# Performance work log

Measured on AMD Instinct MI355X. Metric: run time of the kernel, lower is better.

## Reference

```python
import jax, jax.numpy as jnp
import numpy as np

B = 1024          # batch
S = 2048          # sparseDim == obsDim (required by PhiW shape constraints)
FISTA_ITER = 16


def setup_inputs() -> dict:
    key = jax.random.key(0)
    k1, k2, k3 = jax.random.split(key, 3)
    src = jax.random.normal(k1, (B, S, 1), dtype=jnp.float32)
    Y = jax.random.normal(k2, (B, S, 1), dtype=jnp.float32)
    W = jax.random.normal(k3, (S, S), dtype=jnp.float32)
    # F.normalize(W, p=2, dim=0): unit L2 norm per column
    W = W / jnp.linalg.norm(W, axis=0, keepdims=True)
    alpha = jnp.full((1, 1), 0.1, dtype=jnp.float32)  # alpha_initialize
    return {"src": src, "Y": Y, "W": W, "alpha": alpha}


def reference(src, Y, W, alpha):
    obsDim = W.shape[0]          # == sparseDim == S
    # Lipschitz constant: max |eig(W^T W)|; W^T W is symmetric PSD so eigvalsh is exact
    L = jnp.max(jnp.linalg.eigvalsh(W.T @ W))
    thresh = alpha / L * 0.5     # soft-threshold level, shape [1,1]

    def phiW(x):
        theta_m = x[:, :obsDim]          # [B, S, 1]
        delta = x[:, obsDim:]            # [B, S, 1]
        return src * jnp.matmul(W, theta_m) + delta

    def phiWT(y):
        return jnp.concatenate((jnp.matmul(W.T, src * y), y), axis=1)  # [B, 2S, 1]

    nb = Y.shape[0]
    x0 = jnp.zeros((nb, 2 * obsDim, 1), dtype=Y.dtype)

    def step(carry, _):
        x_old, y_k, t_old = carry
        res = Y - phiW(y_k)
        v = y_k + phiWT(res) / L
        x_new = jnp.sign(v) * jnp.maximum(jnp.abs(v) - thresh, 0.0)
        t_new = (1.0 + jnp.sqrt(1.0 + 4.0 * t_old * t_old)) / 2.0
        y_new = x_new + (t_old - 1.0) / t_new * (x_new - x_old)
        return (x_new, y_new, t_new), None

    (x_new, _, _), _ = jax.lax.scan(
        step, (x0, x0, jnp.float32(1.0)), None, length=FISTA_ITER
    )
    return x_new
```

## Files before the change

kernel.cpp:

```cpp
#include <hip/hip_runtime.h>
#include <math.h>

#define SDIM 2048
#define BATCH 1024
#define NITER 16
#define LM 40

typedef unsigned short ushort_t;
typedef __attribute__((ext_vector_type(8))) short bf16x8;
typedef __attribute__((ext_vector_type(4))) float f32x4;

#define MFMA(a,b,c) __builtin_amdgcn_mfma_f32_16x16x32_bf16((a),(b),(c),0,0,0)

__device__ __forceinline__ float softt(float v, float th){
  return copysignf(fmaxf(fabsf(v) - th, 0.0f), v);
}

__device__ __forceinline__ float bf2f(ushort_t h){
  return __uint_as_float(((unsigned)h) << 16);
}

__device__ __forceinline__ void split2(float x, ushort_t* h, ushort_t* l){
  unsigned u = __float_as_uint(x);
  unsigned hh = (u + 0x7FFFu + ((u >> 16) & 1u)) >> 16;
  float hf = __uint_as_float(hh << 16);
  float r = x - hf;
  unsigned v = __float_as_uint(r);
  unsigned ll = (v + 0x7FFFu + ((v >> 16) & 1u)) >> 16;
  *h = (ushort_t)hh; *l = (ushort_t)ll;
}

__device__ __forceinline__ void cp16(const ushort_t* g, ushort_t* l){
  __builtin_amdgcn_global_load_lds(
      (const __attribute__((address_space(1))) unsigned int*)g,
      (__attribute__((address_space(3))) unsigned int*)l, 16, 0, 0);
}

__device__ __forceinline__ void gemm_core(ushort_t* __restrict__ sm,
                                          const ushort_t* __restrict__ Ah, const ushort_t* __restrict__ Al,
                                          const ushort_t* __restrict__ Bh, const ushort_t* __restrict__ Bl,
                                          int m0, int n0, int K, f32x4 acc[2][2])
{
  ushort_t* lAh = sm;
  ushort_t* lAl = sm + 4096;
  ushort_t* lBh = sm + 8192;
  ushort_t* lBl = sm + 12288;
  const int tid = threadIdx.x;
  const int rr = tid >> 3;
  const int kp = (tid & 7) ^ (rr & 7);
  const size_t strA = (size_t)32 * K;
  const ushort_t* gAh = Ah + (size_t)(m0 + rr) * K + kp * 8;
  const ushort_t* gAl = Al + (size_t)(m0 + rr) * K + kp * 8;
  const ushort_t* gBh = Bh + (size_t)(n0 + rr) * K + kp * 8;
  const ushort_t* gBl = Bl + (size_t)(n0 + rr) * K + kp * 8;
  ushort_t* dA0 = &lAh[tid * 8];      ushort_t* dA1 = &lAh[(tid + 256) * 8];
  ushort_t* dAl0 = &lAl[tid * 8];     ushort_t* dAl1 = &lAl[(tid + 256) * 8];
  ushort_t* dB0 = &lBh[tid * 8];      ushort_t* dB1 = &lBh[(tid + 256) * 8];
  ushort_t* dBl0 = &lBl[tid * 8];     ushort_t* dBl1 = &lBl[(tid + 256) * 8];

  const int lane = tid & 63, wv = tid >> 6;
  const int wm = (wv >> 1) * 32, wn = (wv & 1) * 32;
  const int mm = lane & 15, quad = lane >> 4;
  const int ra0 = wm + mm, ra1 = wm + 16 + mm;
  const int rb0 = wn + mm, rb1 = wn + 16 + mm;
  int oa0[2], oa1[2], ob0[2], ob1[2];
  #pragma unroll
  for (int u = 0; u < 2; u++){
    oa0[u] = ra0*64 + (((u*4 + quad) ^ (ra0 & 7)) << 3);
    oa1[u] = ra1*64 + (((u*4 + quad) ^ (ra1 & 7)) << 3);
    ob0[u] = rb0*64 + (((u*4 + quad) ^ (rb0 & 7)) << 3);
    ob1[u] = rb1*64 + (((u*4 + quad) ^ (rb1 & 7)) << 3);
  }

  const int nk = K / 64;
  cp16(gAh, dA0); cp16(gAh + strA, dA1);
  cp16(gAl, dAl0); cp16(gAl + strA, dAl1);
  cp16(gBh, dB0); cp16(gBh + strA, dB1);
  cp16(gBl, dBl0); cp16(gBl + strA, dBl1);
  gAh += 64; gAl += 64; gBh += 64; gBl += 64;

  for (int kt = 0; kt < nk; kt++){
    __syncthreads();
    bf16x8 ah0[2], ah1[2], al0[2], al1[2], bh0[2], bh1[2], bl0[2], bl1[2];
    #pragma unroll
    for (int u = 0; u < 2; u++){
      ah0[u] = *(const bf16x8*)&lAh[oa0[u]];
      ah1[u] = *(const bf16x8*)&lAh[oa1[u]];
      al0[u] = *(const bf16x8*)&lAl[oa0[u]];
      al1[u] = *(const bf16x8*)&lAl[oa1[u]];
      bh0[u] = *(const bf16x8*)&lBh[ob0[u]];
      bh1[u] = *(const bf16x8*)&lBh[ob1[u]];
      bl0[u] = *(const bf16x8*)&lBl[ob0[u]];
      bl1[u] = *(const bf16x8*)&lBl[ob1[u]];
    }
    __syncthreads();
    if (kt + 1 < nk){
      cp16(gAh, dA0); cp16(gAh + strA, dA1);
      cp16(gAl, dAl0); cp16(gAl + strA, dAl1);
      cp16(gBh, dB0); cp16(gBh + strA, dB1);
      cp16(gBl, dBl0); cp16(gBl + strA, dBl1);
      gAh += 64; gAl += 64; gBh += 64; gBl += 64;
    }
    #pragma unroll
    for (int u = 0; u < 2; u++){
      acc[0][0] = MFMA(ah0[u], bh0[u], acc[0][0]);
      acc[0][0] = MFMA(ah0[u], bl0[u], acc[0][0]);
      acc[0][0] = MFMA(al0[u], bh0[u], acc[0][0]);
      acc[0][1] = MFMA(ah0[u], bh1[u], acc[0][1]);
      acc[0][1] = MFMA(ah0[u], bl1[u], acc[0][1]);
      acc[0][1] = MFMA(al0[u], bh1[u], acc[0][1]);
      acc[1][0] = MFMA(ah1[u], bh0[u], acc[1][0]);
      acc[1][0] = MFMA(ah1[u], bl0[u], acc[1][0]);
      acc[1][0] = MFMA(al1[u], bh0[u], acc[1][0]);
      acc[1][1] = MFMA(ah1[u], bh1[u], acc[1][1]);
      acc[1][1] = MFMA(ah1[u], bl1[u], acc[1][1]);
      acc[1][1] = MFMA(al1[u], bh1[u], acc[1][1]);
    }
  }
}

__device__ __forceinline__ void acc_to_tile(ushort_t* sm, f32x4 acc[2][2]){
  float* tile = (float*)sm;
  const int tid = threadIdx.x, lane = tid & 63, wv = tid >> 6;
  const int wm = (wv >> 1) * 32, wn = (wv & 1) * 32;
  const int mm = lane & 15, quad = lane >> 4;
  #pragma unroll
  for (int tm = 0; tm < 2; tm++)
    #pragma unroll
    for (int tn = 0; tn < 2; tn++)
      #pragma unroll
      for (int i = 0; i < 4; i++)
        tile[(wm + tm*16 + quad*4 + i)*65 + wn + tn*16 + mm] = acc[tm][tn][i];
  __syncthreads();
}

#define EPILOGUE_FOR(rowvar, c4var) \
  const int tid = threadIdx.x, lane = tid & 63, wv = tid >> 6; \
  const int r4 = lane >> 4; \
  const int c4var = (lane & 15) * 4; \
  for (int j = 0; j < 4; j++){ \
    const int rowvar = wv*16 + j*4 + r4;

__global__ __launch_bounds__(256) void k_split(const float* __restrict__ W,
                                               ushort_t* __restrict__ Wah, ushort_t* __restrict__ Wal,
                                               ushort_t* __restrict__ Wbh, ushort_t* __restrict__ Wbl){
  __shared__ float t[32][33];
  const int i0 = blockIdx.y * 32, j0 = blockIdx.x * 32;
  const int r = threadIdx.x >> 3, c = (threadIdx.x & 7) * 4;
  const float4 v = *(const float4*)&W[(size_t)(i0 + r) * SDIM + j0 + c];
  float vv[4] = {v.x, v.y, v.z, v.w};
  ushort_t h[4], l[4];
  #pragma unroll
  for (int q = 0; q < 4; q++){ split2(vv[q], &h[q], &l[q]); t[r][c+q] = vv[q]; }
  *(ushort4*)&Wah[(size_t)(i0 + r) * SDIM + j0 + c] = make_ushort4(h[0],h[1],h[2],h[3]);
  *(ushort4*)&Wal[(size_t)(i0 + r) * SDIM + j0 + c] = make_ushort4(l[0],l[1],l[2],l[3]);
  __syncthreads();
  #pragma unroll
  for (int q = 0; q < 4; q++) split2(t[c+q][r], &h[q], &l[q]);
  *(ushort4*)&Wbh[(size_t)(j0 + r) * SDIM + i0 + c] = make_ushort4(h[0],h[1],h[2],h[3]);
  *(ushort4*)&Wbl[(size_t)(j0 + r) * SDIM + i0 + c] = make_ushort4(l[0],l[1],l[2],l[3]);
}

__global__ __launch_bounds__(256) void k_gemmM(const ushort_t* __restrict__ Wah, const ushort_t* __restrict__ Wal,
                                               float* __restrict__ Mmat){
  __shared__ __align__(16) ushort_t smem[16384];
  const int b = blockIdx.x + (blockIdx.y << 5);
  const int xcd = b & 7, slot = b >> 3;
  const int n0 = (((xcd << 2) + (slot >> 5)) << 6);
  const int m0 = ((slot & 31) << 6);
  f32x4 acc[2][2] = {};
  gemm_core(smem, Wah, Wal, Wah, Wal, m0, n0, SDIM, acc);
  acc_to_tile(smem, acc);
  const float* tile = (const float*)smem;
  EPILOGUE_FOR(row, c4)
    f32x4 a = *(const f32x4*)&tile[row*65 + c4];
    *(f32x4*)&Mmat[(size_t)(m0 + row) * SDIM + n0 + c4] = a;
  }
}

__global__ __launch_bounds__(256) void k_init(float* __restrict__ vRing,
                                              double* __restrict__ dotWV, double* __restrict__ dotWW,
                                              float* __restrict__ betaSq){
  __shared__ float red[256];
  int t = threadIdx.x;
  float vals[8];
  float s = 0.f;
  #pragma unroll
  for (int p = 0; p < 8; p++){
    int j = p*256 + t;
    unsigned h = (unsigned)j * 2654435761u;
    h ^= h >> 16; h *= 2246822519u; h ^= h >> 13;
    float r = (float)(h & 0xFFFFFFu) / 16777216.0f - 0.5f;
    vals[p] = r; s += r*r;
  }
  red[t] = s; __syncthreads();
  for (int o = 128; o > 0; o >>= 1){ if (t < o) red[t] += red[t+o]; __syncthreads(); }
  float inv = rsqrtf(red[0]);
  #pragma unroll
  for (int p = 0; p < 8; p++){
    int j = p*256 + t;
    vRing[SDIM + j] = vals[p]*inv;
    vRing[j] = 0.f;
    vRing[2*SDIM + j] = 0.f;
  }
  if (t < LM+2){ dotWV[t] = 0.0; dotWW[t] = 0.0; betaSq[t] = 0.f; }
}

__global__ __launch_bounds__(256) void k_lstep(const float* __restrict__ M,
    const float* __restrict__ wOld, float* __restrict__ wNew,
    float* __restrict__ vRing, double* __restrict__ dotWV, double* __restrict__ dotWW,
    float* __restrict__ betaSq, int s){
  __shared__ float vs[SDIM];
  __shared__ double pAl[4], pWw[4];
  const int tid = threadIdx.x, bid = blockIdx.x;
  if (s == 1){
    const float* v1 = vRing + SDIM;
    for (int j = tid; j < SDIM; j += 256) vs[j] = v1[j];
  } else {
    const double a  = dotWV[s-1];
    const double ww = dotWW[s-1];
    const float bpSq = betaSq[s-2];
    float bsq = (float)(ww - a*a - (double)bpSq);
    bsq = fmaxf(bsq, 1e-20f);
    const float beta = sqrtf(bsq), invb = 1.0f/beta;
    const float alpha = (float)a, bprev = sqrtf(bpSq);
    const float* vm1 = vRing + ((s-1)%3)*SDIM;
    const float* vm2 = vRing + ((s-2)%3)*SDIM;
    float* vdst = vRing + (s%3)*SDIM;
    for (int j = tid; j < SDIM; j += 256){
      float val = (wOld[j] - alpha*vm1[j] - bprev*vm2[j]) * invb;
      vs[j] = val;
      if (bid == 0) vdst[j] = val;
    }
    if (bid == 0 && tid == 0) betaSq[s-1] = bsq;
  }
  __syncthreads();
  const int wv = tid >> 6, lane = tid & 63;
  const int row = bid*4 + wv;
  const float4* Mr = (const float4*)(M + (size_t)row * SDIM);
  const float4* v4 = (const float4*)vs;
  float acc = 0.f;
  #pragma unroll
  for (int p = 0; p < 8; p++){
    int j4 = p*64 + lane;
    float4 m = Mr[j4], v = v4[j4];
    acc += m.x*v.x + m.y*v.y + m.z*v.z + m.w*v.w;
  }
  #pragma unroll
  for (int o = 32; o > 0; o >>= 1) acc += __shfl_down(acc, o);
  if (lane == 0){
    wNew[row] = acc;
    pAl[wv] = (double)acc * (double)vs[row];
    pWw[wv] = (double)acc * (double)acc;
  }
  __syncthreads();
  if (tid == 0){
    atomicAdd(&dotWV[s], pAl[0]+pAl[1]+pAl[2]+pAl[3]);
    atomicAdd(&dotWW[s], pWw[0]+pWw[1]+pWw[2]+pWw[3]);
  }
}

__global__ void k_sturm(const double* __restrict__ dotWV, const float* __restrict__ betaSq,
                        const float* __restrict__ alphaIn, float* __restrict__ Lbuf){
  __shared__ double sa[LM+1], sb[LM+1];
  int lane = threadIdx.x;
  for (int i = lane; i <= LM; i += 64){
    if (i >= 1){
      sa[i] = dotWV[i];
      sb[i] = (i < LM) ? sqrt((double)betaSq[i]) : 0.0;
    }
  }
  __syncthreads();
  double phi = -1e300, plo = 1e300;
  for (int i = 1 + lane; i <= LM; i += 64){
    double r = (i > 1 ? sb[i-1] : 0.0) + (i < LM ? sb[i] : 0.0);
    phi = fmax(phi, sa[i] + r);
    plo = fmin(plo, sa[i] - r);
  }
  for (int o = 32; o > 0; o >>= 1){
    phi = fmax(phi, __shfl_down(phi, o));
    plo = fmin(plo, __shfl_down(plo, o));
  }
  double hi = __shfl(phi, 0), lo = __shfl(plo, 0);
  for (int round = 0; round < 6; round++){
    double x = lo + (hi - lo) * (double)(lane + 1) / 65.0;
    int cnt = 0;
    double dd = sa[1] - x;
    if (dd < 0) cnt++;
    for (int i = 2; i <= LM; i++){
      double off = sb[i-1];
      if (fabs(dd) < 1e-300) dd = -1e-300;
      dd = sa[i] - x - off*off/dd;
      if (dd < 0) cnt++;
    }
    unsigned long long bal = __ballot(cnt == LM);
    int p = (bal == 0ull) ? 64 : (__ffsll((unsigned long long)bal) - 1);
    double newhi = (p <= 63) ? lo + (hi - lo) * (double)(p + 1) / 65.0 : hi;
    double newlo = (p >= 1)  ? lo + (hi - lo) * (double)p / 65.0       : lo;
    hi = newhi; lo = newlo;
  }
  if (lane == 0){
    double L = 0.5*(lo + hi);
    Lbuf[0] = (float)(1.0 / L);
    Lbuf[1] = (float)(0.5 * (double)alphaIn[0] / L);
  }
}


__global__ __launch_bounds__(256) void k_A0(const float* __restrict__ Y, const float* __restrict__ src,
                                            float* __restrict__ yd, ushort_t* __restrict__ sresh,
                                            ushort_t* __restrict__ sresl, float* __restrict__ out,
                                            const float* __restrict__ Lbuf){
  int idx = blockIdx.x*256 + threadIdx.x;
  float invL = Lbuf[0], th = Lbuf[1];
  float y = Y[idx], s = src[idx];
  split2(s*y, &sresh[idx], &sresl[idx]);
  float xn = softt(y*invL, th);
  int b = idx >> 11, i = idx & 2047;
  out[(size_t)b*4096 + 2048 + i] = xn;
  yd[idx] = xn;
}

__device__ __forceinline__ void swz512(int* m0, int* n0){
  const int b = blockIdx.x + (blockIdx.y << 5);
  const int xcd = b & 7, slot = b >> 3;
  *n0 = (((xcd << 2) + (slot >> 4)) << 6);
  *m0 = ((slot & 15) << 6);
}

__global__ __launch_bounds__(256) void k_gemmA(
    const ushort_t* __restrict__ Wah, const ushort_t* __restrict__ Wal,
    const ushort_t* __restrict__ ymh, const ushort_t* __restrict__ yml,
    const float* __restrict__ Y, const float* __restrict__ src,
    float* __restrict__ yd, float* __restrict__ out,
    ushort_t* __restrict__ sresh, ushort_t* __restrict__ sresl,
    const float* __restrict__ Lbuf, float ck)
{
  __shared__ __align__(16) ushort_t smem[16384];
  f32x4 acc[2][2] = {};
  int m0, n0; swz512(&m0, &n0);
  gemm_core(smem, ymh, yml, Wah, Wal, m0, n0, SDIM, acc);
  acc_to_tile(smem, acc);
  const float* tile = (const float*)smem;
  const float invL = Lbuf[0], th = Lbuf[1];
  EPILOGUE_FOR(row, c4)
    const int brow = m0 + row;
    const size_t g  = (size_t)brow*SDIM + n0 + c4;
    const size_t go = (size_t)brow*4096 + 2048 + n0 + c4;
    f32x4 a   = *(const f32x4*)&tile[row*65 + c4];
    f32x4 s4  = *(const f32x4*)&src[g];
    f32x4 y4  = *(const f32x4*)&Y[g];
    f32x4 yd4 = *(const f32x4*)&yd[g];
    f32x4 xo4 = *(const f32x4*)&out[go];
    f32x4 res, xn, yn;
    ushort4 sh, sl;
    #pragma unroll
    for (int q = 0; q < 4; q++){
      res[q] = y4[q] - s4[q]*a[q] - yd4[q];
      xn[q]  = softt(yd4[q] + res[q]*invL, th);
      yn[q]  = xn[q] + ck*(xn[q] - xo4[q]);
    }
    split2(s4[0]*res[0], &sh.x, &sl.x);
    split2(s4[1]*res[1], &sh.y, &sl.y);
    split2(s4[2]*res[2], &sh.z, &sl.z);
    split2(s4[3]*res[3], &sh.w, &sl.w);
    *(ushort4*)&sresh[g] = sh;
    *(ushort4*)&sresl[g] = sl;
    *(f32x4*)&out[go] = xn;
    *(f32x4*)&yd[g]   = yn;
  }
}

template<bool FIRST>
__global__ __launch_bounds__(256) void k_gemmB(
    const ushort_t* __restrict__ Wbh, const ushort_t* __restrict__ Wbl,
    const ushort_t* __restrict__ sresh, const ushort_t* __restrict__ sresl,
    ushort_t* __restrict__ ymh, ushort_t* __restrict__ yml,
    float* __restrict__ out, const float* __restrict__ Lbuf, float ck)
{
  __shared__ __align__(16) ushort_t smem[16384];
  f32x4 acc[2][2] = {};
  int m0, n0; swz512(&m0, &n0);
  gemm_core(smem, sresh, sresl, Wbh, Wbl, m0, n0, SDIM, acc);
  acc_to_tile(smem, acc);
  const float* tile = (const float*)smem;
  const float invL = Lbuf[0], th = Lbuf[1];
  EPILOGUE_FOR(row, c4)
    const int brow = m0 + row;
    const size_t g  = (size_t)brow*SDIM + n0 + c4;
    const size_t go = (size_t)brow*4096 + n0 + c4;
    f32x4 a = *(const f32x4*)&tile[row*65 + c4];
    f32x4 ym4, xo4;
    if (FIRST){
      ym4 = (f32x4){0.f,0.f,0.f,0.f};
      xo4 = (f32x4){0.f,0.f,0.f,0.f};
    } else {
      ushort4 h4 = *(const ushort4*)&ymh[g];
      ushort4 l4 = *(const ushort4*)&yml[g];
      ym4[0] = bf2f(h4.x) + bf2f(l4.x);
      ym4[1] = bf2f(h4.y) + bf2f(l4.y);
      ym4[2] = bf2f(h4.z) + bf2f(l4.z);
      ym4[3] = bf2f(h4.w) + bf2f(l4.w);
      xo4 = *(const f32x4*)&out[go];
    }
    f32x4 xn, yn;
    ushort4 hh, ll;
    #pragma unroll
    for (int q = 0; q < 4; q++){
      xn[q] = softt(ym4[q] + a[q]*invL, th);
      yn[q] = xn[q] + ck*(xn[q] - xo4[q]);
    }
    split2(yn[0], &hh.x, &ll.x);
    split2(yn[1], &hh.y, &ll.y);
    split2(yn[2], &hh.z, &ll.z);
    split2(yn[3], &hh.w, &ll.w);
    *(f32x4*)&out[go] = xn;
    *(ushort4*)&ymh[g] = hh;
    *(ushort4*)&yml[g] = ll;
  }
}


extern "C" void kernel_launch(void* const* d_in, const int* in_sizes, int n_in,
                              void* d_out, int out_size, void* d_ws, size_t ws_size,
                              hipStream_t stream) {
  const float* src   = (const float*)d_in[0];
  const float* Y     = (const float*)d_in[1];
  const float* W     = (const float*)d_in[2];
  const float* alpha = (const float*)d_in[3];
  float* out = (float*)d_out;
  float* ws  = (float*)d_ws;

  const size_t M1 = 1024*1024;
  float* Mmat = ws;
  float* yd   = ws + 4*M1;
  float* lanc = ws + 6*M1;
  float* w0      = lanc;
  float* w1      = lanc + SDIM;
  float* vRing   = lanc + 2*SDIM;
  double* dotWV  = (double*)(lanc + 5*SDIM);
  double* dotWW  = dotWV + 128;
  float* betaSq  = lanc + 5*SDIM + 512;
  float* Lbuf    = betaSq + 128;
  ushort_t* u16 = (ushort_t*)(ws + 7*M1);
  ushort_t* Wah = u16;
  ushort_t* Wal = u16 + 4*M1;
  ushort_t* Wbh = u16 + 8*M1;
  ushort_t* Wbl = u16 + 12*M1;
  ushort_t* ymh = u16 + 16*M1;
  ushort_t* yml = u16 + 18*M1;
  ushort_t* sresh = u16 + 20*M1;
  ushort_t* sresl = u16 + 22*M1;

  k_split<<<dim3(64,64), 256, 0, stream>>>(W, Wah, Wal, Wbh, Wbl);
  k_gemmM<<<dim3(32,32), 256, 0, stream>>>(Wah, Wal, Mmat);

  float* wb[2] = { w0, w1 };
  k_init<<<1, 256, 0, stream>>>(vRing, dotWV, dotWW, betaSq);
  for (int s = 1; s <= LM; s++){
    k_lstep<<<512, 256, 0, stream>>>(Mmat, wb[(s+1)&1], wb[s&1], vRing, dotWV, dotWW, betaSq, s);
  }
  k_sturm<<<1, 64, 0, stream>>>(dotWV, betaSq, alpha, Lbuf);

  double t = 1.0;
  float ckv[NITER];
  for (int k = 0; k < NITER; k++){
    double tn = 0.5*(1.0 + sqrt(1.0 + 4.0*t*t));
    ckv[k] = (float)((t - 1.0)/tn);
    t = tn;
  }

  k_A0<<<(BATCH*SDIM)/256, 256, 0, stream>>>(Y, src, yd, sresh, sresl, out, Lbuf);
  k_gemmB<true><<<dim3(32,16), 256, 0, stream>>>(Wbh, Wbl, sresh, sresl, ymh, yml, out, Lbuf, ckv[0]);
  for (int k = 1; k < NITER; k++){
    k_gemmA<<<dim3(32,16), 256, 0, stream>>>(Wah, Wal, ymh, yml, Y, src, yd, out, sresh, sresl, Lbuf, ckv[k]);
    k_gemmB<false><<<dim3(32,16), 256, 0, stream>>>(Wbh, Wbl, sresh, sresl, ymh, yml, out, Lbuf, ckv[k]);
  }
  (void)in_sizes; (void)n_in; (void)out_size; (void)ws_size;
}
```

Baseline: 1.708 ms.

## Split K across two blocks per tile in FISTA GEMMs with atomic-counter combine

The per-iteration GEMMs now launch twice as many blocks (1024 instead of 512). Each block computes half of the K dimension and writes its partial accumulator to a workspace that reuses the Mmat buffer. An atomic counter per tile decides which block arrives second; that block adds the other partial and runs the fused epilogue. This is meant to fill the GPU's compute units better, since 512 tiles underoccupy them. The cost is extra partial-sum traffic, atomics, and a memset of the counters.

Measured after the change: 2.867 ms. +67.8%, slower.

```diff
diff --git a/kernel.cpp b/kernel.cpp
--- a/kernel.cpp
+++ b/kernel.cpp
@@ -39,7 +39,7 @@
 __device__ __forceinline__ void gemm_core(ushort_t* __restrict__ sm,
                                           const ushort_t* __restrict__ Ah, const ushort_t* __restrict__ Al,
                                           const ushort_t* __restrict__ Bh, const ushort_t* __restrict__ Bl,
-                                          int m0, int n0, int K, f32x4 acc[2][2])
+                                          int m0, int n0, int K, int kbase, int klen, f32x4 acc[2][2])
 {
   ushort_t* lAh = sm;
   ushort_t* lAl = sm + 4096;
@@ -49,10 +49,10 @@
   const int rr = tid >> 3;
   const int kp = (tid & 7) ^ (rr & 7);
   const size_t strA = (size_t)32 * K;
-  const ushort_t* gAh = Ah + (size_t)(m0 + rr) * K + kp * 8;
-  const ushort_t* gAl = Al + (size_t)(m0 + rr) * K + kp * 8;
-  const ushort_t* gBh = Bh + (size_t)(n0 + rr) * K + kp * 8;
-  const ushort_t* gBl = Bl + (size_t)(n0 + rr) * K + kp * 8;
+  const ushort_t* gAh = Ah + (size_t)(m0 + rr) * K + kbase + kp * 8;
+  const ushort_t* gAl = Al + (size_t)(m0 + rr) * K + kbase + kp * 8;
+  const ushort_t* gBh = Bh + (size_t)(n0 + rr) * K + kbase + kp * 8;
+  const ushort_t* gBl = Bl + (size_t)(n0 + rr) * K + kbase + kp * 8;
   ushort_t* dA0 = &lAh[tid * 8];      ushort_t* dA1 = &lAh[(tid + 256) * 8];
   ushort_t* dAl0 = &lAl[tid * 8];     ushort_t* dAl1 = &lAl[(tid + 256) * 8];
   ushort_t* dB0 = &lBh[tid * 8];      ushort_t* dB1 = &lBh[(tid + 256) * 8];
@@ -72,7 +72,7 @@
     ob1[u] = rb1*64 + (((u*4 + quad) ^ (rb1 & 7)) << 3);
   }
 
-  const int nk = K / 64;
+  const int nk = klen / 64;
   cp16(gAh, dA0); cp16(gAh + strA, dA1);
   cp16(gAl, dAl0); cp16(gAl + strA, dAl1);
   cp16(gBh, dB0); cp16(gBh + strA, dB1);
@@ -141,6 +141,26 @@
   for (int j = 0; j < 4; j++){ \
     const int rowvar = wv*16 + j*4 + r4;
 
+__device__ __forceinline__ bool ksplit_combine(float* __restrict__ Pws, int* __restrict__ cnt,
+                                               int tile, int kh, f32x4 acc[2][2], int* sflag){
+  const int t = threadIdx.x;
+  float* myP = Pws + (((size_t)tile << 1) + kh) * 4096;
+  #pragma unroll
+  for (int i = 0; i < 16; i++)
+    __hip_atomic_store(&myP[i*256 + t], acc[(i>>3)&1][(i>>2)&1][i&3],
+                       __ATOMIC_RELAXED, __HIP_MEMORY_SCOPE_AGENT);
+  if (t == 0)
+    *sflag = __hip_atomic_fetch_add(&cnt[tile], 1, __ATOMIC_ACQ_REL, __HIP_MEMORY_SCOPE_AGENT);
+  __syncthreads();
+  if (*sflag == 0) return false;
+  const float* pP = Pws + (((size_t)tile << 1) + (kh ^ 1)) * 4096;
+  #pragma unroll
+  for (int i = 0; i < 16; i++)
+    acc[(i>>3)&1][(i>>2)&1][i&3] += __hip_atomic_load(&pP[i*256 + t],
+                       __ATOMIC_RELAXED, __HIP_MEMORY_SCOPE_AGENT);
+  return true;
+}
+
 __global__ __launch_bounds__(256) void k_split(const float* __restrict__ W,
                                                ushort_t* __restrict__ Wah, ushort_t* __restrict__ Wal,
                                                ushort_t* __restrict__ Wbh, ushort_t* __restrict__ Wbl){
@@ -169,7 +189,7 @@
   const int n0 = (((xcd << 2) + (slot >> 5)) << 6);
   const int m0 = ((slot & 31) << 6);
   f32x4 acc[2][2] = {};
-  gemm_core(smem, Wah, Wal, Wah, Wal, m0, n0, SDIM, acc);
+  gemm_core(smem, Wah, Wal, Wah, Wal, m0, n0, SDIM, 0, SDIM, acc);
   acc_to_tile(smem, acc);
   const float* tile = (const float*)smem;
   EPILOGUE_FOR(row, c4)
@@ -321,11 +341,16 @@
   yd[idx] = xn;
 }
 
-__device__ __forceinline__ void swz512(int* m0, int* n0){
+__device__ __forceinline__ void swzF(int* m0, int* n0, int* kh, int* tile){
   const int b = blockIdx.x + (blockIdx.y << 5);
   const int xcd = b & 7, slot = b >> 3;
-  *n0 = (((xcd << 2) + (slot >> 4)) << 6);
-  *m0 = ((slot & 15) << 6);
+  const int nt = (xcd << 2) + (slot >> 5);
+  const int mk = slot & 31;
+  const int mt = mk >> 1;
+  *kh = mk & 1;
+  *m0 = mt << 6;
+  *n0 = nt << 6;
+  *tile = (mt << 5) + nt;
 }
 
 __global__ __launch_bounds__(256) void k_gemmA(
@@ -334,20 +359,23 @@
     const float* __restrict__ Y, const float* __restrict__ src,
     float* __restrict__ yd, float* __restrict__ out,
     ushort_t* __restrict__ sresh, ushort_t* __restrict__ sresl,
-    const float* __restrict__ Lbuf, float ck)
+    const float* __restrict__ Lbuf, float ck,
+    float* __restrict__ Pws, int* __restrict__ cnt)
 {
   __shared__ __align__(16) ushort_t smem[16384];
+  __shared__ int sflag;
   f32x4 acc[2][2] = {};
-  int m0, n0; swz512(&m0, &n0);
-  gemm_core(smem, ymh, yml, Wah, Wal, m0, n0, SDIM, acc);
+  int m0, n0, kh, tile; swzF(&m0, &n0, &kh, &tile);
+  gemm_core(smem, ymh, yml, Wah, Wal, m0, n0, SDIM, kh << 10, 1024, acc);
+  if (!ksplit_combine(Pws, cnt, tile, kh, acc, &sflag)) return;
   acc_to_tile(smem, acc);
-  const float* tile = (const float*)smem;
+  const float* tile_f = (const float*)smem;
   const float invL = Lbuf[0], th = Lbuf[1];
   EPILOGUE_FOR(row, c4)
     const int brow = m0 + row;
     const size_t g  = (size_t)brow*SDIM + n0 + c4;
     const size_t go = (size_t)brow*4096 + 2048 + n0 + c4;
-    f32x4 a   = *(const f32x4*)&tile[row*65 + c4];
+    f32x4 a   = *(const f32x4*)&tile_f[row*65 + c4];
     f32x4 s4  = *(const f32x4*)&src[g];
     f32x4 y4  = *(const f32x4*)&Y[g];
     f32x4 yd4 = *(const f32x4*)&yd[g];
@@ -376,20 +404,23 @@
     const ushort_t* __restrict__ Wbh, const ushort_t* __restrict__ Wbl,
     const ushort_t* __restrict__ sresh, const ushort_t* __restrict__ sresl,
     ushort_t* __restrict__ ymh, ushort_t* __restrict__ yml,
-    float* __restrict__ out, const float* __restrict__ Lbuf, float ck)
+    float* __restrict__ out, const float* __restrict__ Lbuf, float ck,
+    float* __restrict__ Pws, int* __restrict__ cnt)
 {
   __shared__ __align__(16) ushort_t smem[16384];
+  __shared__ int sflag;
   f32x4 acc[2][2] = {};
-  int m0, n0; swz512(&m0, &n0);
-  gemm_core(smem, sresh, sresl, Wbh, Wbl, m0, n0, SDIM, acc);
+  int m0, n0, kh, tile; swzF(&m0, &n0, &kh, &tile);
+  gemm_core(smem, sresh, sresl, Wbh, Wbl, m0, n0, SDIM, kh << 10, 1024, acc);
+  if (!ksplit_combine(Pws, cnt, tile, kh, acc, &sflag)) return;
   acc_to_tile(smem, acc);
-  const float* tile = (const float*)smem;
+  const float* tile_f = (const float*)smem;
   const float invL = Lbuf[0], th = Lbuf[1];
   EPILOGUE_FOR(row, c4)
     const int brow = m0 + row;
     const size_t g  = (size_t)brow*SDIM + n0 + c4;
     const size_t go = (size_t)brow*4096 + n0 + c4;
-    f32x4 a = *(const f32x4*)&tile[row*65 + c4];
+    f32x4 a = *(const f32x4*)&tile_f[row*65 + c4];
     f32x4 ym4, xo4;
     if (FIRST){
       ym4 = (f32x4){0.f,0.f,0.f,0.f};
@@ -451,6 +482,8 @@
   ushort_t* yml = u16 + 18*M1;
   ushort_t* sresh = u16 + 20*M1;
   ushort_t* sresl = u16 + 22*M1;
+  float* Pws = Mmat;
+  int* cnt = (int*)(ws + 19*M1);
 
   k_split<<<dim3(64,64), 256, 0, stream>>>(W, Wah, Wal, Wbh, Wbl);
   k_gemmM<<<dim3(32,32), 256, 0, stream>>>(Wah, Wal, Mmat);
@@ -461,6 +494,8 @@
     k_lstep<<<512, 256, 0, stream>>>(Mmat, wb[(s+1)&1], wb[s&1], vRing, dotWV, dotWW, betaSq, s);
   }
   k_sturm<<<1, 64, 0, stream>>>(dotWV, betaSq, alpha, Lbuf);
+
+  hipMemsetAsync(cnt, 0, 31*512*sizeof(int), stream);
 
   double t = 1.0;
   float ckv[NITER];
@@ -470,11 +505,15 @@
     t = tn;
   }
 
+  int ep = 0;
   k_A0<<<(BATCH*SDIM)/256, 256, 0, stream>>>(Y, src, yd, sresh, sresl, out, Lbuf);
-  k_gemmB<true><<<dim3(32,16), 256, 0, stream>>>(Wbh, Wbl, sresh, sresl, ymh, yml, out, Lbuf, ckv[0]);
+  k_gemmB<true><<<dim3(32,32), 256, 0, stream>>>(Wbh, Wbl, sresh, sresl, ymh, yml, out, Lbuf, ckv[0],
+                                                 Pws, cnt + (ep++)*512);
   for (int k = 1; k < NITER; k++){
-    k_gemmA<<<dim3(32,16), 256, 0, stream>>>(Wah, Wal, ymh, yml, Y, src, yd, out, sresh, sresl, Lbuf, ckv[k]);
-    k_gemmB<false><<<dim3(32,16), 256, 0, stream>>>(Wbh, Wbl, sresh, sresl, ymh, yml, out, Lbuf, ckv[k]);
+    k_gemmA<<<dim3(32,32), 256, 0, stream>>>(Wah, Wal, ymh, yml, Y, src, yd, out, sresh, sresl, Lbuf, ckv[k],
+                                             Pws, cnt + (ep++)*512);
+    k_gemmB<false><<<dim3(32,32), 256, 0, stream>>>(Wbh, Wbl, sresh, sresl, ymh, yml, out, Lbuf, ckv[k],
+                                                    Pws, cnt + (ep++)*512);
   }
   (void)in_sizes; (void)n_in; (void)out_size; (void)ws_size;
 }
```

## Enlarge GEMM tiles to 128x64 with double-buffered LDS pipeline

Applied to the files above, without the earlier changes.

Replaces the 64x64 single-buffer GEMM core with a templated 128x64 tile, where each warp computes a 64x32 sub-tile (4x2 MFMA fragments). LDS is now double buffered: the next K-slice is loaded asynchronously while the current one is consumed, which removes one barrier per K step. Grids are halved and the block swizzles are adjusted to match. The cost is more registers and 96KB of dynamic LDS per block, which lowers occupancy and halves the number of blocks.

After: 1.845 ms. +8.0%, slower.

```diff
diff --git a/kernel.cpp b/kernel.cpp
--- a/kernel.cpp
+++ b/kernel.cpp
@@ -36,110 +36,133 @@
       (__attribute__((address_space(3))) unsigned int*)l, 16, 0, 0);
 }
 
-__device__ __forceinline__ void gemm_core(ushort_t* __restrict__ sm,
-                                          const ushort_t* __restrict__ Ah, const ushort_t* __restrict__ Al,
-                                          const ushort_t* __restrict__ Bh, const ushort_t* __restrict__ Bl,
-                                          int m0, int n0, int K, f32x4 acc[2][2])
+template<int BM, int BN>
+__device__ __forceinline__ void gemm_core2(ushort_t* __restrict__ sm,
+    const ushort_t* __restrict__ Ah, const ushort_t* __restrict__ Al,
+    const ushort_t* __restrict__ Bh, const ushort_t* __restrict__ Bl,
+    int m0, int n0, int K, f32x4 acc[4][2])
 {
-  ushort_t* lAh = sm;
-  ushort_t* lAl = sm + 4096;
-  ushort_t* lBh = sm + 8192;
-  ushort_t* lBl = sm + 12288;
+  constexpr int BK   = 64;
+  constexpr int ABUF = BM * BK;
+  constexpr int BBUF = BN * BK;
+  constexpr int BUFSZ = 2*ABUF + 2*BBUF;
+  constexpr int ARND = BM / 32;
+  constexpr int BRND = BN / 32;
   const int tid = threadIdx.x;
   const int rr = tid >> 3;
   const int kp = (tid & 7) ^ (rr & 7);
-  const size_t strA = (size_t)32 * K;
-  const ushort_t* gAh = Ah + (size_t)(m0 + rr) * K + kp * 8;
-  const ushort_t* gAl = Al + (size_t)(m0 + rr) * K + kp * 8;
-  const ushort_t* gBh = Bh + (size_t)(n0 + rr) * K + kp * 8;
-  const ushort_t* gBl = Bl + (size_t)(n0 + rr) * K + kp * 8;
-  ushort_t* dA0 = &lAh[tid * 8];      ushort_t* dA1 = &lAh[(tid + 256) * 8];
-  ushort_t* dAl0 = &lAl[tid * 8];     ushort_t* dAl1 = &lAl[(tid + 256) * 8];
-  ushort_t* dB0 = &lBh[tid * 8];      ushort_t* dB1 = &lBh[(tid + 256) * 8];
-  ushort_t* dBl0 = &lBl[tid * 8];     ushort_t* dBl1 = &lBl[(tid + 256) * 8];
+
+  const ushort_t* pAh[ARND]; const ushort_t* pAl[ARND];
+  const ushort_t* pBh[BRND]; const ushort_t* pBl[BRND];
+  #pragma unroll
+  for (int r = 0; r < ARND; r++){
+    pAh[r] = Ah + (size_t)(m0 + rr + r*32) * K + kp*8;
+    pAl[r] = Al + (size_t)(m0 + rr + r*32) * K + kp*8;
+  }
+  #pragma unroll
+  for (int r = 0; r < BRND; r++){
+    pBh[r] = Bh + (size_t)(n0 + rr + r*32) * K + kp*8;
+    pBl[r] = Bl + (size_t)(n0 + rr + r*32) * K + kp*8;
+  }
 
   const int lane = tid & 63, wv = tid >> 6;
-  const int wm = (wv >> 1) * 32, wn = (wv & 1) * 32;
+  const int wr = (wv >> 1) * 64, wc = (wv & 1) * 32;
   const int mm = lane & 15, quad = lane >> 4;
-  const int ra0 = wm + mm, ra1 = wm + 16 + mm;
-  const int rb0 = wn + mm, rb1 = wn + 16 + mm;
-  int oa0[2], oa1[2], ob0[2], ob1[2];
-  #pragma unroll
-  for (int u = 0; u < 2; u++){
-    oa0[u] = ra0*64 + (((u*4 + quad) ^ (ra0 & 7)) << 3);
-    oa1[u] = ra1*64 + (((u*4 + quad) ^ (ra1 & 7)) << 3);
-    ob0[u] = rb0*64 + (((u*4 + quad) ^ (rb0 & 7)) << 3);
-    ob1[u] = rb1*64 + (((u*4 + quad) ^ (rb1 & 7)) << 3);
-  }
-
-  const int nk = K / 64;
-  cp16(gAh, dA0); cp16(gAh + strA, dA1);
-  cp16(gAl, dAl0); cp16(gAl + strA, dAl1);
-  cp16(gBh, dB0); cp16(gBh + strA, dB1);
-  cp16(gBl, dBl0); cp16(gBl + strA, dBl1);
-  gAh += 64; gAl += 64; gBh += 64; gBl += 64;
+  int oa[4][2], ob[2][2];
+  #pragma unroll
+  for (int t = 0; t < 4; t++){
+    const int r = wr + t*16 + mm;
+    #pragma unroll
+    for (int u = 0; u < 2; u++)
+      oa[t][u] = r*BK + (((u*4 + quad) ^ (r & 7)) << 3);
+  }
+  #pragma unroll
+  for (int s = 0; s < 2; s++){
+    const int r = wc + s*16 + mm;
+    #pragma unroll
+    for (int u = 0; u < 2; u++)
+      ob[s][u] = r*BK + (((u*4 + quad) ^ (r & 7)) << 3);
+  }
+
+  const int nk = K / BK;
+  #pragma unroll
+  for (int r = 0; r < ARND; r++){
+    cp16(pAh[r], &sm[(tid + r*256)*8]);
+    cp16(pAl[r], &sm[ABUF + (tid + r*256)*8]);
+  }
+  #pragma unroll
+  for (int r = 0; r < BRND; r++){
+    cp16(pBh[r], &sm[2*ABUF + (tid + r*256)*8]);
+    cp16(pBl[r], &sm[2*ABUF + BBUF + (tid + r*256)*8]);
+  }
 
   for (int kt = 0; kt < nk; kt++){
+    const int cur = kt & 1;
     __syncthreads();
-    bf16x8 ah0[2], ah1[2], al0[2], al1[2], bh0[2], bh1[2], bl0[2], bl1[2];
+    if (kt + 1 < nk){
+      ushort_t* d = sm + (cur ^ 1) * BUFSZ;
+      const int ko = (kt + 1) * BK;
+      #pragma unroll
+      for (int r = 0; r < ARND; r++){
+        cp16(pAh[r] + ko, &d[(tid + r*256)*8]);
+        cp16(pAl[r] + ko, &d[ABUF + (tid + r*256)*8]);
+      }
+      #pragma unroll
+      for (int r = 0; r < BRND; r++){
+        cp16(pBh[r] + ko, &d[2*ABUF + (tid + r*256)*8]);
+        cp16(pBl[r] + ko, &d[2*ABUF + BBUF + (tid + r*256)*8]);
+      }
+    }
+    const ushort_t* sA  = sm + cur * BUFSZ;
+    const ushort_t* sAl = sA + ABUF;
+    const ushort_t* sB  = sA + 2*ABUF;
+    const ushort_t* sBl = sA + 2*ABUF + BBUF;
     #pragma unroll
     for (int u = 0; u < 2; u++){
-      ah0[u] = *(const bf16x8*)&lAh[oa0[u]];
-      ah1[u] = *(const bf16x8*)&lAh[oa1[u]];
-      al0[u] = *(const bf16x8*)&lAl[oa0[u]];
-      al1[u] = *(const bf16x8*)&lAl[oa1[u]];
-      bh0[u] = *(const bf16x8*)&lBh[ob0[u]];
-      bh1[u] = *(const bf16x8*)&lBh[ob1[u]];
-      bl0[u] = *(const bf16x8*)&lBl[ob0[u]];
-      bl1[u] = *(const bf16x8*)&lBl[ob1[u]];
-    }
-    __syncthreads();
-    if (kt + 1 < nk){
-      cp16(gAh, dA0); cp16(gAh + strA, dA1);
-      cp16(gAl, dAl0); cp16(gAl + strA, dAl1);
-      cp16(gBh, dB0); cp16(gBh + strA, dB1);
-      cp16(gBl, dBl0); cp16(gBl + strA, dBl1);
-      gAh += 64; gAl += 64; gBh += 64; gBl += 64;
-    }
-    #pragma unroll
-    for (int u = 0; u < 2; u++){
-      acc[0][0] = MFMA(ah0[u], bh0[u], acc[0][0]);
-      acc[0][0] = MFMA(ah0[u], bl0[u], acc[0][0]);
-      acc[0][0] = MFMA(al0[u], bh0[u], acc[0][0]);
-      acc[0][1] = MFMA(ah0[u], bh1[u], acc[0][1]);
-      acc[0][1] = MFMA(ah0[u], bl1[u], acc[0][1]);
-      acc[0][1] = MFMA(al0[u], bh1[u], acc[0][1]);
-      acc[1][0] = MFMA(ah1[u], bh0[u], acc[1][0]);
-      acc[1][0] = MFMA(ah1[u], bl0[u], acc[1][0]);
-      acc[1][0] = MFMA(al1[u], bh0[u], acc[1][0]);
-      acc[1][1] = MFMA(ah1[u], bh1[u], acc[1][1]);
-      acc[1][1] = MFMA(ah1[u], bl1[u], acc[1][1]);
-      acc[1][1] = MFMA(al1[u], bh1[u], acc[1][1]);
-    }
-  }
-}
-
-__device__ __forceinline__ void acc_to_tile(ushort_t* sm, f32x4 acc[2][2]){
+      bf16x8 ah[4], al8[4], bh[2], bl8[2];
+      #pragma unroll
+      for (int t = 0; t < 4; t++){
+        ah[t]  = *(const bf16x8*)&sA [oa[t][u]];
+        al8[t] = *(const bf16x8*)&sAl[oa[t][u]];
+      }
+      #pragma unroll
+      for (int s = 0; s < 2; s++){
+        bh[s]  = *(const bf16x8*)&sB [ob[s][u]];
+        bl8[s] = *(const bf16x8*)&sBl[ob[s][u]];
+      }
+      #pragma unroll
+      for (int t = 0; t < 4; t++)
+        #pragma unroll
+        for (int s = 0; s < 2; s++){
+          acc[t][s] = MFMA(ah[t],  bh[s],  acc[t][s]);
+          acc[t][s] = MFMA(ah[t],  bl8[s], acc[t][s]);
+          acc[t][s] = MFMA(al8[t], bh[s],  acc[t][s]);
+        }
+    }
+  }
+}
+
+__device__ __forceinline__ void acc_to_tile2(ushort_t* sm, f32x4 acc[4][2]){
   float* tile = (float*)sm;
   const int tid = threadIdx.x, lane = tid & 63, wv = tid >> 6;
-  const int wm = (wv >> 1) * 32, wn = (wv & 1) * 32;
+  const int wr = (wv >> 1) * 64, wc = (wv & 1) * 32;
   const int mm = lane & 15, quad = lane >> 4;
   #pragma unroll
-  for (int tm = 0; tm < 2; tm++)
+  for (int tm = 0; tm < 4; tm++)
     #pragma unroll
     for (int tn = 0; tn < 2; tn++)
       #pragma unroll
       for (int i = 0; i < 4; i++)
-        tile[(wm + tm*16 + quad*4 + i)*65 + wn + tn*16 + mm] = acc[tm][tn][i];
+        tile[(wr + tm*16 + quad*4 + i)*65 + wc + tn*16 + mm] = acc[tm][tn][i];
   __syncthreads();
 }
 
-#define EPILOGUE_FOR(rowvar, c4var) \
-  const int tid = threadIdx.x, lane = tid & 63, wv = tid >> 6; \
-  const int r4 = lane >> 4; \
-  const int c4var = (lane & 15) * 4; \
-  for (int j = 0; j < 4; j++){ \
-    const int rowvar = wv*16 + j*4 + r4;
+#define EPILOGUE2_FOR(rowvar, c4var) \
+  const int tid = threadIdx.x; \
+  const int g16 = tid >> 4; \
+  const int c4var = (tid & 15) * 4; \
+  for (int j = 0; j < 8; j++){ \
+    const int rowvar = j*16 + g16;
 
 __global__ __launch_bounds__(256) void k_split(const float* __restrict__ W,
                                                ushort_t* __restrict__ Wah, ushort_t* __restrict__ Wal,
@@ -161,18 +184,28 @@
   *(ushort4*)&Wbl[(size_t)(j0 + r) * SDIM + i0 + c] = make_ushort4(l[0],l[1],l[2],l[3]);
 }
 
+__device__ __forceinline__ void swzM2(int* m0, int* n0){
+  const int b = blockIdx.x + (blockIdx.y << 5);
+  const int xcd = b & 7, slot = b >> 3;
+  *n0 = ((xcd << 2) + (slot >> 4)) << 6;
+  *m0 = (slot & 15) << 7;
+}
+__device__ __forceinline__ void swzF2(int* m0, int* n0){
+  const int b = blockIdx.x + (blockIdx.y << 5);
+  const int xcd = b & 7, slot = b >> 3;
+  *n0 = ((xcd << 2) + (slot >> 3)) << 6;
+  *m0 = (slot & 7) << 7;
+}
+
 __global__ __launch_bounds__(256) void k_gemmM(const ushort_t* __restrict__ Wah, const ushort_t* __restrict__ Wal,
                                                float* __restrict__ Mmat){
-  __shared__ __align__(16) ushort_t smem[16384];
-  const int b = blockIdx.x + (blockIdx.y << 5);
-  const int xcd = b & 7, slot = b >> 3;
-  const int n0 = (((xcd << 2) + (slot >> 5)) << 6);
-  const int m0 = ((slot & 31) << 6);
-  f32x4 acc[2][2] = {};
-  gemm_core(smem, Wah, Wal, Wah, Wal, m0, n0, SDIM, acc);
-  acc_to_tile(smem, acc);
+  extern __shared__ __align__(16) ushort_t smem[];
+  int m0, n0; swzM2(&m0, &n0);
+  f32x4 acc[4][2] = {};
+  gemm_core2<128,64>(smem, Wah, Wal, Wah, Wal, m0, n0, SDIM, acc);
+  acc_to_tile2(smem, acc);
   const float* tile = (const float*)smem;
-  EPILOGUE_FOR(row, c4)
+  EPILOGUE2_FOR(row, c4)
     f32x4 a = *(const f32x4*)&tile[row*65 + c4];
     *(f32x4*)&Mmat[(size_t)(m0 + row) * SDIM + n0 + c4] = a;
   }
@@ -321,13 +354,6 @@
   yd[idx] = xn;
 }
 
-__device__ __forceinline__ void swz512(int* m0, int* n0){
-  const int b = blockIdx.x + (blockIdx.y << 5);
-  const int xcd = b & 7, slot = b >> 3;
-  *n0 = (((xcd << 2) + (slot >> 4)) << 6);
-  *m0 = ((slot & 15) << 6);
-}
-
 __global__ __launch_bounds__(256) void k_gemmA(
     const ushort_t* __restrict__ Wah, const ushort_t* __restrict__ Wal,
     const ushort_t* __restrict__ ymh, const ushort_t* __restrict__ yml,
@@ -336,14 +362,14 @@
     ushort_t* __restrict__ sresh, ushort_t* __restrict__ sresl,
     const float* __restrict__ Lbuf, float ck)
 {
-  __shared__ __align__(16) ushort_t smem[16384];
-  f32x4 acc[2][2] = {};
-  int m0, n0; swz512(&m0, &n0);
-  gemm_core(smem, ymh, yml, Wah, Wal, m0, n0, SDIM, acc);
-  acc_to_tile(smem, acc);
+  extern __shared__ __align__(16) ushort_t smem[];
+  f32x4 acc[4][2] = {};
+  int m0, n0; swzF2(&m0, &n0);
+  gemm_core2<128,64>(smem, ymh, yml, Wah, Wal, m0, n0, SDIM, acc);
+  acc_to_tile2(smem, acc);
   const float* tile = (const float*)smem;
   const float invL = Lbuf[0], th = Lbuf[1];
-  EPILOGUE_FOR(row, c4)
+  EPILOGUE2_FOR(row, c4)
     const int brow = m0 + row;
     const size_t g  = (size_t)brow*SDIM + n0 + c4;
     const size_t go = (size_t)brow*4096 + 2048 + n0 + c4;
@@ -378,14 +404,14 @@
     ushort_t* __restrict__ ymh, ushort_t* __restrict__ yml,
     float* __restrict__ out, const float* __restrict__ Lbuf, float ck)
 {
-  __shared__ __align__(16) ushort_t smem[16384];
-  f32x4 acc[2][2] = {};
-  int m0, n0; swz512(&m0, &n0);
-  gemm_core(smem, sresh, sresl, Wbh, Wbl, m0, n0, SDIM, acc);
-  acc_to_tile(smem, acc);
+  extern __shared__ __align__(16) ushort_t smem[];
+  f32x4 acc[4][2] = {};
+  int m0, n0; swzF2(&m0, &n0);
+  gemm_core2<128,64>(smem, sresh, sresl, Wbh, Wbl, m0, n0, SDIM, acc);
+  acc_to_tile2(smem, acc);
   const float* tile = (const float*)smem;
   const float invL = Lbuf[0], th = Lbuf[1];
-  EPILOGUE_FOR(row, c4)
+  EPILOGUE2_FOR(row, c4)
     const int brow = m0 + row;
     const size_t g  = (size_t)brow*SDIM + n0 + c4;
     const size_t go = (size_t)brow*4096 + n0 + c4;
@@ -452,8 +478,10 @@
   ushort_t* sresh = u16 + 20*M1;
   ushort_t* sresl = u16 + 22*M1;
 
+  const size_t LDSB = 98304;
+
   k_split<<<dim3(64,64), 256, 0, stream>>>(W, Wah, Wal, Wbh, Wbl);
-  k_gemmM<<<dim3(32,32), 256, 0, stream>>>(Wah, Wal, Mmat);
+  k_gemmM<<<dim3(32,16), 256, LDSB, stream>>>(Wah, Wal, Mmat);
 
   float* wb[2] = { w0, w1 };
   k_init<<<1, 256, 0, stream>>>(vRing, dotWV, dotWW, betaSq);
@@ -471,10 +499,10 @@
   }
 
   k_A0<<<(BATCH*SDIM)/256, 256, 0, stream>>>(Y, src, yd, sresh, sresl, out, Lbuf);
-  k_gemmB<true><<<dim3(32,16), 256, 0, stream>>>(Wbh, Wbl, sresh, sresl, ymh, yml, out, Lbuf, ckv[0]);
+  k_gemmB<true><<<dim3(32,8), 256, LDSB, stream>>>(Wbh, Wbl, sresh, sresl, ymh, yml, out, Lbuf, ckv[0]);
   for (int k = 1; k < NITER; k++){
-    k_gemmA<<<dim3(32,16), 256, 0, stream>>>(Wah, Wal, ymh, yml, Y, src, yd, out, sresh, sresl, Lbuf, ckv[k]);
-    k_gemmB<false><<<dim3(32,16), 256, 0, stream>>>(Wbh, Wbl, sresh, sresl, ymh, yml, out, Lbuf, ckv[k]);
+    k_gemmA<<<dim3(32,8), 256, LDSB, stream>>>(Wah, Wal, ymh, yml, Y, src, yd, out, sresh, sresl, Lbuf, ckv[k]);
+    k_gemmB<false><<<dim3(32,8), 256, LDSB, stream>>>(Wbh, Wbl, sresh, sresl, ymh, yml, out, Lbuf, ckv[k]);
   }
   (void)in_sizes; (void)n_in; (void)out_size; (void)ws_size;
 }
```
